# Kernel tuning notes

Measured on AMD Instinct MI355X. Metric: run time of the kernel, lower is better.

## Reference

```python
import jax, jax.numpy as jnp
import numpy as np
import math

HIDDEN = 2048
NUM_HEADS = 16
HEAD_DIM = 128
ROPE_BASE = 10000.0


def _rope_emb(seq_len, dim, dtype):
    # freqs[i, j] = i * base**(-2j/dim); emb = concat(freqs, freqs) -> [S, dim]
    inv_freq = 1.0 / (ROPE_BASE ** (jnp.arange(0, dim, 2, dtype=jnp.float32) / dim))
    t = jnp.arange(seq_len, dtype=jnp.float32)
    freqs = t[:, None] * inv_freq[None, :]            # [S, dim/2]
    return jnp.concatenate([freqs, freqs], axis=-1).astype(dtype)  # [S, dim]


def _apply_rope(x, emb):
    # x: [B, H, S, D]; emb: [S, D] broadcast over batch and heads.
    # Roll-based rotary variant from the source: x*cos + roll(x, 1, -1)*sin
    e = emb[None, None, :, :]
    return x * jnp.cos(e) + jnp.roll(x, shift=1, axis=-1) * jnp.sin(e)


def setup_inputs() -> dict:
    key = jax.random.key(0)
    ks = jax.random.split(key, 5)
    B, S = 2, 2048
    scale = 1.0 / math.sqrt(HIDDEN)
    return {
        "hidden_states": jax.random.normal(ks[0], (B, S, HIDDEN), dtype=jnp.float32),
        "Wq": jax.random.normal(ks[1], (HIDDEN, HIDDEN), dtype=jnp.float32) * scale,
        "Wk": jax.random.normal(ks[2], (HIDDEN, HIDDEN), dtype=jnp.float32) * scale,
        "Wv": jax.random.normal(ks[3], (HIDDEN, HIDDEN), dtype=jnp.float32) * scale,
        "Wo": jax.random.normal(ks[4], (HIDDEN, HIDDEN), dtype=jnp.float32) * scale,
    }


def reference(hidden_states, Wq, Wk, Wv, Wo):
    B, S, _ = hidden_states.shape
    H, D = NUM_HEADS, HEAD_DIM

    def split_heads(x):
        return x.reshape(B, S, H, D).transpose(0, 2, 1, 3)  # [B,H,S,D]

    q = split_heads(hidden_states @ Wq)
    k = split_heads(hidden_states @ Wk)
    v = split_heads(hidden_states @ Wv)

    emb = _rope_emb(S, D, hidden_states.dtype)  # [S, D]
    q = _apply_rope(q, emb)
    k = _apply_rope(k, emb)

    scores = jnp.einsum("bhqd,bhkd->bhqk", q, k) / math.sqrt(D)  # [B,H,S,S]
    probs = jax.nn.softmax(scores, axis=-1)
    ctx = jnp.einsum("bhqk,bhkd->bhqd", probs, v)  # [B,H,S,D]
    ctx = ctx.transpose(0, 2, 1, 3).reshape(B, S, H * D)
    return ctx @ Wo
```

## Files before the change

### kernel.cpp

```cpp
#include <hip/hip_runtime.h>

#define HIDDEN 2048
#define SEQ    2048
#define BATCH  2
#define NHEAD  16
#define HDIM   128

typedef __attribute__((ext_vector_type(4))) int    i32x4;
typedef __attribute__((ext_vector_type(4))) float  f32x4;
typedef __attribute__((ext_vector_type(8))) __bf16 bf16x8;

__device__ __forceinline__ unsigned short f2bf(float f) {
    return __builtin_bit_cast(unsigned short, (__bf16)f);
}
__device__ __forceinline__ float bf2f(unsigned short h) {
    unsigned u = ((unsigned)h) << 16;
    return __builtin_bit_cast(float, u);
}
__device__ __forceinline__ void gl_lds16(const unsigned short* g, unsigned short* l) {
    __builtin_amdgcn_global_load_lds(
        (const __attribute__((address_space(1))) unsigned int*)g,
        (__attribute__((address_space(3))) unsigned int*)l, 16, 0, 0);
}

__global__ void k_rope_tables(float* __restrict__ ctab, float* __restrict__ stab) {
    int idx = blockIdx.x * 256 + threadIdx.x;
    int t = idx >> 6, i = idx & 63;
    float inv = expf(-(float)i * 0.14391156831212793f);
    float ang = (float)t * inv;
    ctab[idx] = cosf(ang);
    stab[idx] = sinf(ang);
}

__global__ void k_cvt_bf16(const float* __restrict__ in, unsigned short* __restrict__ out, int n4) {
    int idx = blockIdx.x * blockDim.x + threadIdx.x;
    if (idx < n4) {
        float4 v = ((const float4*)in)[idx];
        ushort4 o;
        o.x = f2bf(v.x); o.y = f2bf(v.y); o.z = f2bf(v.z); o.w = f2bf(v.w);
        ((ushort4*)out)[idx] = o;
    }
}

__global__ void k_transcvt4(const float* __restrict__ W0, const float* __restrict__ W1,
                            const float* __restrict__ W2, const float* __restrict__ W3,
                            unsigned short* __restrict__ O0, unsigned short* __restrict__ O1,
                            unsigned short* __restrict__ O2, unsigned short* __restrict__ O3) {
    __shared__ float tile[32][33];
    int z = blockIdx.z;
    const float* in = (z == 0) ? W0 : (z == 1) ? W1 : (z == 2) ? W2 : W3;
    unsigned short* out = (z == 0) ? O0 : (z == 1) ? O1 : (z == 2) ? O2 : O3;
    float scl = (z == 0) ? 0.12751743f : 1.0f;
    int tx = threadIdx.x, ty = threadIdx.y;
    int x = blockIdx.x * 32 + tx, y0 = blockIdx.y * 32;
#pragma unroll
    for (int i = 0; i < 4; i++)
        tile[ty + i * 8][tx] = in[(size_t)(y0 + ty + i * 8) * HIDDEN + x];
    __syncthreads();
    int x2 = blockIdx.y * 32 + tx, y2 = blockIdx.x * 32;
#pragma unroll
    for (int i = 0; i < 4; i++)
        out[(size_t)(y2 + ty + i * 8) * HIDDEN + x2] = f2bf(tile[tx][ty + i * 8] * scl);
}

template <int OUTB>
__global__ __launch_bounds__(512, 1) void k_gemm256(
    const unsigned short* __restrict__ A,
    const unsigned short* __restrict__ B0, const unsigned short* __restrict__ B1,
    const unsigned short* __restrict__ B2,
    void* __restrict__ C0, void* __restrict__ C1, void* __restrict__ C2,
    int K)
{
    __shared__ __align__(16) unsigned short S[3 * 24576];
    const int nwg = gridDim.x;
    int id = blockIdx.x;
    int wg = (id & 7) * (nwg >> 3) + (id >> 3);
    const int z = wg >> 8;
    const int my = (wg >> 4) & 15, nx = wg & 15;
    const unsigned short* Bm = (z == 0) ? B0 : (z == 1 ? B1 : B2);
    void* Cv = (z == 0) ? C0 : (z == 1 ? C1 : C2);
    const int m0 = my * 256, n0 = nx * 128;
    const int tid = threadIdx.x, l = tid & 63, w = tid >> 6;
    const int wm = w >> 1, wn = w & 1;
    const int lr = l & 15, lg = l >> 4;

    const unsigned short* sg[6];
    int so[6];
#pragma unroll
    for (int j = 0; j < 4; j++) {
        int c = tid + j * 512, row = c >> 3, k8 = c & 7;
        sg[j] = A + (size_t)(m0 + row) * K + ((k8 ^ (row & 7)) * 8);
        so[j] = row * 64 + k8 * 8;
    }
#pragma unroll
    for (int j = 0; j < 2; j++) {
        int c = tid + j * 512, row = c >> 3, k8 = c & 7;
        sg[4 + j] = Bm + (size_t)(n0 + row) * K + ((k8 ^ (row & 7)) * 8);
        so[4 + j] = 16384 + row * 64 + k8 * 8;
    }

    f32x4 acc[4][4] = {};

    auto stage = [&](int t) {
        unsigned short* buf = &S[(t % 3) * 24576];
        const int ko = t * 64;
#pragma unroll
        for (int j = 0; j < 6; j++) gl_lds16(sg[j] + ko, &buf[so[j]]);
    };
    auto compute = [&](int t) {
        const unsigned short* buf = &S[(t % 3) * 24576];
        const unsigned short* bb = buf + 16384;
        const int xk0 = (lg ^ (lr & 7)) * 8, xk1 = ((4 + lg) ^ (lr & 7)) * 8;
        i32x4 af0[4], af1[4], bf0[4], bf1[4];
#pragma unroll
        for (int i = 0; i < 4; i++) {
            int R = (wm * 64 + i * 16 + lr) * 64;
            af0[i] = *(const i32x4*)&buf[R + xk0];
            af1[i] = *(const i32x4*)&buf[R + xk1];
        }
#pragma unroll
        for (int j = 0; j < 4; j++) {
            int R = (wn * 64 + j * 16 + lr) * 64;
            bf0[j] = *(const i32x4*)&bb[R + xk0];
            bf1[j] = *(const i32x4*)&bb[R + xk1];
        }
        __builtin_amdgcn_s_setprio(1);
#pragma unroll
        for (int i = 0; i < 4; i++)
#pragma unroll
            for (int j = 0; j < 4; j++)
                acc[i][j] = __builtin_amdgcn_mfma_f32_16x16x32_bf16(
                    __builtin_bit_cast(bf16x8, af0[i]),
                    __builtin_bit_cast(bf16x8, bf0[j]), acc[i][j], 0, 0, 0);
#pragma unroll
        for (int i = 0; i < 4; i++)
#pragma unroll
            for (int j = 0; j < 4; j++)
                acc[i][j] = __builtin_amdgcn_mfma_f32_16x16x32_bf16(
                    __builtin_bit_cast(bf16x8, af1[i]),
                    __builtin_bit_cast(bf16x8, bf1[j]), acc[i][j], 0, 0, 0);
        __builtin_amdgcn_s_setprio(0);
    };

    const int nt = K / 64;
    stage(0); stage(1);
    for (int t = 0; t < nt - 1; ++t) {
        asm volatile("s_waitcnt vmcnt(6)" ::: "memory");
        __builtin_amdgcn_s_barrier();
        __builtin_amdgcn_sched_barrier(0);
        if (t < nt - 2) stage(t + 2);
        compute(t);
    }
    asm volatile("s_waitcnt vmcnt(0)" ::: "memory");
    __builtin_amdgcn_s_barrier();
    __builtin_amdgcn_sched_barrier(0);
    compute(nt - 1);

#pragma unroll
    for (int i = 0; i < 4; i++)
#pragma unroll
        for (int j = 0; j < 4; j++)
#pragma unroll
            for (int r = 0; r < 4; r++) {
                int m = m0 + wm * 64 + i * 16 + lg * 4 + r;
                int n = n0 + wn * 64 + j * 16 + lr;
                float v = acc[i][j][r];
                if (OUTB) ((unsigned short*)Cv)[(size_t)m * 2048 + n] = f2bf(v);
                else      ((float*)Cv)[(size_t)m * 2048 + n] = v;
            }
}

__global__ void k_rope(unsigned short* __restrict__ Q, unsigned short* __restrict__ Kb,
                       const float* __restrict__ ctab, const float* __restrict__ stab)
{
    const int tid = threadIdx.x, l = tid & 63, w = tid >> 6;
    int hr = blockIdx.x * 4 + w;
    unsigned short* X = blockIdx.y ? Kb : Q;
    int bt = hr >> 4, h = hr & 15, t = bt & (SEQ - 1);
    size_t base = (size_t)bt * HIDDEN + h * HDIM;
    int d0 = l * 2;
    ushort2 xv = *(const ushort2*)&X[base + d0];
    float x0 = bf2f(xv.x), x1 = bf2f(xv.y);
    float prev = __shfl(x1, (l + 63) & 63);
    int i0 = d0 & 63, i1 = (d0 + 1) & 63;
    float c0 = ctab[t * 64 + i0], s0 = stab[t * 64 + i0];
    float c1 = ctab[t * 64 + i1], s1 = stab[t * 64 + i1];
    ushort2 ov;
    ov.x = f2bf(x0 * c0 + prev * s0);
    ov.y = f2bf(x1 * c1 + x0 * s1);
    *(ushort2*)&X[base + d0] = ov;
}

__global__ void k_vtrans(const unsigned short* __restrict__ V, unsigned short* __restrict__ Vt)
{
    __shared__ unsigned short tile[32][33];
    int z = blockIdx.z;
    int b = z >> 4, h = z & 15;
    int tx = threadIdx.x, ty = threadIdx.y;
    int d0 = blockIdx.x * 32, t0 = blockIdx.y * 32;
    const size_t ibase = (size_t)b * SEQ * HIDDEN + h * HDIM;
#pragma unroll
    for (int i = 0; i < 4; i++)
        tile[ty + i * 8][tx] = V[ibase + (size_t)(t0 + ty + i * 8) * HIDDEN + d0 + tx];
    __syncthreads();
    const size_t obase = (size_t)z * HDIM * SEQ;
#pragma unroll
    for (int i = 0; i < 4; i++)
        Vt[obase + (size_t)(d0 + ty + i * 8) * SEQ + t0 + tx] = tile[tx][ty + i * 8];
}

__global__ __launch_bounds__(512) void k_attn(
    const unsigned short* __restrict__ Q, const unsigned short* __restrict__ K,
    const unsigned short* __restrict__ Vt, unsigned short* __restrict__ ctx)
{
    __shared__ __align__(16) unsigned short Klds[2][64 * 128];
    __shared__ __align__(16) unsigned short Vlds[2][128 * 64];
    __shared__ __align__(16) unsigned short Plds[8][32 * 64];
    const int tid = threadIdx.x, l = tid & 63, w = tid >> 6;
    const int lr = l & 15, lg = l >> 4;
    const int bid = blockIdx.x;
    const int sX = bid >> 3;
    const int bh = (bid & 7) * 4 + (sX >> 3);
    const int q0 = (sX & 7) * 256;
    const int b = bh >> 4, h = bh & 15;

    i32x4 qf[2][4];
#pragma unroll
    for (int qh = 0; qh < 2; qh++) {
        const unsigned short* qbase =
            Q + (size_t)(b * SEQ + q0 + w * 32 + qh * 16 + lr) * HIDDEN + h * HDIM + lg * 8;
#pragma unroll
        for (int c = 0; c < 4; c++) qf[qh][c] = *(const i32x4*)(qbase + c * 32);
    }

    const unsigned short* kg[2];
    const unsigned short* vg[2];
    int kl[2], vl[2];
#pragma unroll
    for (int c = 0; c < 2; c++) {
        int cc = tid + c * 512;
        {   int row = cc >> 4, ch = cc & 15, sch = ch ^ (row & 7);
            kg[c] = K + (size_t)(b * SEQ + row) * HIDDEN + h * HDIM + sch * 8;
            kl[c] = cc * 8; }
        {   int row = cc >> 3, ch = cc & 7, sch = ch ^ (row & 7);
            vg[c] = Vt + (size_t)(bh * HDIM + row) * SEQ + sch * 8;
            vl[c] = cc * 8; }
    }

    auto stage = [&](int t, int bsel) {
        const size_t ko = (size_t)t * 64;
#pragma unroll
        for (int c = 0; c < 2; c++) {
            gl_lds16(kg[c] + ko * HIDDEN, &Klds[bsel][kl[c]]);
            gl_lds16(vg[c] + ko,          &Vlds[bsel][vl[c]]);
        }
    };

    f32x4 acc[2][8] = {};
    float m_run[2] = {-1e30f, -1e30f}, l_run[2] = {0.f, 0.f};

    stage(0, 0);
    const int nt = SEQ / 64;
    for (int t = 0; t < nt; ++t) {
        asm volatile("s_waitcnt vmcnt(0)" ::: "memory");
        __builtin_amdgcn_s_barrier();
        asm volatile("" ::: "memory");
        __builtin_amdgcn_sched_barrier(0);
        if (t + 1 < nt) stage(t + 1, (t + 1) & 1);
        const unsigned short* Kb_ = Klds[t & 1];
        const unsigned short* Vb_ = Vlds[t & 1];

        f32x4 s[4][2];
        __builtin_amdgcn_s_setprio(1);
#pragma unroll
        for (int ks = 0; ks < 4; ks++) {
            s[ks][0] = f32x4{0.f, 0.f, 0.f, 0.f};
            s[ks][1] = f32x4{0.f, 0.f, 0.f, 0.f};
#pragma unroll
            for (int c = 0; c < 4; c++) {
                i32x4 kf = *(const i32x4*)&Kb_[(ks * 16 + lr) * 128 + ((c * 4 + lg) ^ (lr & 7)) * 8];
                s[ks][0] = __builtin_amdgcn_mfma_f32_16x16x32_bf16(
                    __builtin_bit_cast(bf16x8, kf), __builtin_bit_cast(bf16x8, qf[0][c]),
                    s[ks][0], 0, 0, 0);
                s[ks][1] = __builtin_amdgcn_mfma_f32_16x16x32_bf16(
                    __builtin_bit_cast(bf16x8, kf), __builtin_bit_cast(bf16x8, qf[1][c]),
                    s[ks][1], 0, 0, 0);
            }
        }
        __builtin_amdgcn_s_setprio(0);

        float p[2][4][4];
        float fac[2];
        bool need_any = false;
#pragma unroll
        for (int qh = 0; qh < 2; qh++) {
            float mx0 = fmaxf(fmaxf(s[0][qh][0], s[0][qh][1]), fmaxf(s[0][qh][2], s[0][qh][3]));
            float mx1 = fmaxf(fmaxf(s[1][qh][0], s[1][qh][1]), fmaxf(s[1][qh][2], s[1][qh][3]));
            float mx2 = fmaxf(fmaxf(s[2][qh][0], s[2][qh][1]), fmaxf(s[2][qh][2], s[2][qh][3]));
            float mx3 = fmaxf(fmaxf(s[3][qh][0], s[3][qh][1]), fmaxf(s[3][qh][2], s[3][qh][3]));
            float pmax = fmaxf(fmaxf(mx0, mx1), fmaxf(mx2, mx3));
            pmax = fmaxf(pmax, __shfl_xor(pmax, 16));
            pmax = fmaxf(pmax, __shfl_xor(pmax, 32));
            bool need = pmax > m_run[qh] + 8.0f;
            fac[qh] = need ? __builtin_amdgcn_exp2f(m_run[qh] - pmax) : 1.0f;
            float mn = need ? pmax : m_run[qh];
            m_run[qh] = mn;
            float psum = 0.f;
#pragma unroll
            for (int ks = 0; ks < 4; ks++) {
                float e0 = __builtin_amdgcn_exp2f(s[ks][qh][0] - mn);
                float e1 = __builtin_amdgcn_exp2f(s[ks][qh][1] - mn);
                float e2 = __builtin_amdgcn_exp2f(s[ks][qh][2] - mn);
                float e3 = __builtin_amdgcn_exp2f(s[ks][qh][3] - mn);
                p[qh][ks][0] = e0; p[qh][ks][1] = e1;
                p[qh][ks][2] = e2; p[qh][ks][3] = e3;
                psum += (e0 + e1) + (e2 + e3);
            }
            psum += __shfl_xor(psum, 16);
            psum += __shfl_xor(psum, 32);
            l_run[qh] = l_run[qh] * fac[qh] + psum;
            need_any |= need;
        }

        unsigned short* pw = &Plds[w][0];
#pragma unroll
        for (int qh = 0; qh < 2; qh++)
#pragma unroll
            for (int ks = 0; ks < 4; ks++) {
                ushort4 pk;
                pk.x = f2bf(p[qh][ks][0]); pk.y = f2bf(p[qh][ks][1]);
                pk.z = f2bf(p[qh][ks][2]); pk.w = f2bf(p[qh][ks][3]);
                int chunk = ks * 2 + (lg >> 1);
                *(ushort4*)&pw[(qh * 16 + lr) * 64 + ((chunk ^ (lr & 7)) * 8) + (lg & 1) * 4] = pk;
            }

        if (__any((int)need_any)) {
#pragma unroll
            for (int qh = 0; qh < 2; qh++) {
                float facq[4];
#pragma unroll
                for (int r = 0; r < 4; r++) facq[r] = __shfl(fac[qh], lg * 4 + r);
#pragma unroll
                for (int db = 0; db < 8; db++)
#pragma unroll
                    for (int r = 0; r < 4; r++) acc[qh][db][r] *= facq[r];
            }
        }

        __builtin_amdgcn_s_setprio(1);
#pragma unroll
        for (int kk = 0; kk < 2; kk++) {
            i32x4 pf0 = *(const i32x4*)&pw[(lr) * 64 + ((kk * 4 + lg) ^ (lr & 7)) * 8];
            i32x4 pf1 = *(const i32x4*)&pw[(16 + lr) * 64 + ((kk * 4 + lg) ^ (lr & 7)) * 8];
#pragma unroll
            for (int db = 0; db < 8; db++) {
                i32x4 vf = *(const i32x4*)&Vb_[(db * 16 + lr) * 64 + ((kk * 4 + lg) ^ (lr & 7)) * 8];
                acc[0][db] = __builtin_amdgcn_mfma_f32_16x16x32_bf16(
                    __builtin_bit_cast(bf16x8, pf0), __builtin_bit_cast(bf16x8, vf),
                    acc[0][db], 0, 0, 0);
                acc[1][db] = __builtin_amdgcn_mfma_f32_16x16x32_bf16(
                    __builtin_bit_cast(bf16x8, pf1), __builtin_bit_cast(bf16x8, vf),
                    acc[1][db], 0, 0, 0);
            }
        }
        __builtin_amdgcn_s_setprio(0);
    }

#pragma unroll
    for (int qh = 0; qh < 2; qh++) {
        float inv[4];
#pragma unroll
        for (int r = 0; r < 4; r++) inv[r] = 1.0f / __shfl(l_run[qh], lg * 4 + r);
#pragma unroll
        for (int db = 0; db < 8; db++)
#pragma unroll
            for (int r = 0; r < 4; r++) {
                int trow = q0 + w * 32 + qh * 16 + lg * 4 + r;
                ctx[(size_t)(b * SEQ + trow) * HIDDEN + h * HDIM + db * 16 + lr] =
                    f2bf(acc[qh][db][r] * inv[r]);
            }
    }
}

extern "C" void kernel_launch(void* const* d_in, const int* in_sizes, int n_in,
                              void* d_out, int out_size, void* d_ws, size_t ws_size,
                              hipStream_t stream)
{
    (void)in_sizes; (void)n_in; (void)out_size; (void)ws_size;
    const float* X  = (const float*)d_in[0];
    const float* Wq = (const float*)d_in[1];
    const float* Wk = (const float*)d_in[2];
    const float* Wv = (const float*)d_in[3];
    const float* Wo = (const float*)d_in[4];
    float* out = (float*)d_out;
    char* ws = (char*)d_ws;

    unsigned short* Xb  = (unsigned short*)(ws);
    unsigned short* WqT = (unsigned short*)(ws + 16777216);
    unsigned short* WkT = (unsigned short*)(ws + 25165824);
    unsigned short* WvT = (unsigned short*)(ws + 33554432);
    unsigned short* WoT = (unsigned short*)(ws + 41943040);
    unsigned short* Qb  = (unsigned short*)(ws + 50331648);
    unsigned short* Kb  = (unsigned short*)(ws + 67108864);
    unsigned short* Vb  = (unsigned short*)(ws + 83886080);
    unsigned short* Vt  = (unsigned short*)(ws + 100663296);
    unsigned short* Cx  = (unsigned short*)(ws + 117440512);
    float* ctab = (float*)(ws + 134217728);
    float* stab = (float*)(ws + 134742016);

    k_rope_tables<<<512, 256, 0, stream>>>(ctab, stab);
    k_cvt_bf16<<<8192, 256, 0, stream>>>(X, Xb, 2097152);
    k_transcvt4<<<dim3(64, 64, 4), dim3(32, 8), 0, stream>>>(Wq, Wk, Wv, Wo,
                                                             WqT, WkT, WvT, WoT);
    k_gemm256<1><<<768, 512, 0, stream>>>(Xb, WqT, WkT, WvT, Qb, Kb, Vb, 2048);
    k_rope<<<dim3(16384, 2), 256, 0, stream>>>(Qb, Kb, ctab, stab);
    k_vtrans<<<dim3(4, 64, 32), dim3(32, 8), 0, stream>>>(Vb, Vt);
    k_attn<<<256, 512, 0, stream>>>(Qb, Kb, Vt, Cx);
    k_gemm256<0><<<256, 512, 0, stream>>>(Cx, WoT, WoT, WoT, out, out, out, 2048);
}
```

Baseline: 289.6 us.

## Split GEMM main loop into two half-phases interleaving LDS reads, prefetch and MFMA

```diff
diff --git a/kernel.cpp b/kernel.cpp
--- a/kernel.cpp
+++ b/kernel.cpp
@@ -101,19 +101,34 @@
 
     f32x4 acc[4][4] = {};
 
-    auto stage = [&](int t) {
+    auto stage6 = [&](int t) {
         unsigned short* buf = &S[(t % 3) * 24576];
         const int ko = t * 64;
 #pragma unroll
         for (int j = 0; j < 6; j++) gl_lds16(sg[j] + ko, &buf[so[j]]);
     };
-    auto compute = [&](int t) {
+    auto stageH = [&](int t, int h) {
+        unsigned short* buf = &S[(t % 3) * 24576];
+        const int ko = t * 64;
+        gl_lds16(sg[h * 2] + ko,     &buf[so[h * 2]]);
+        gl_lds16(sg[h * 2 + 1] + ko, &buf[so[h * 2 + 1]]);
+        gl_lds16(sg[4 + h] + ko,     &buf[so[4 + h]]);
+    };
+
+    const int nt = K / 64;
+    stage6(0); stage6(1);
+    asm volatile("s_waitcnt vmcnt(6)" ::: "memory");
+    __builtin_amdgcn_s_barrier();
+    __builtin_amdgcn_sched_barrier(0);
+
+    for (int t = 0; t < nt; ++t) {
         const unsigned short* buf = &S[(t % 3) * 24576];
         const unsigned short* bb = buf + 16384;
         const int xk0 = (lg ^ (lr & 7)) * 8, xk1 = ((4 + lg) ^ (lr & 7)) * 8;
-        i32x4 af0[4], af1[4], bf0[4], bf1[4];
-#pragma unroll
-        for (int i = 0; i < 4; i++) {
+        i32x4 af0[2], af1[2], bf0[4], bf1[4];
+
+#pragma unroll
+        for (int i = 0; i < 2; i++) {
             int R = (wm * 64 + i * 16 + lr) * 64;
             af0[i] = *(const i32x4*)&buf[R + xk0];
             af1[i] = *(const i32x4*)&buf[R + xk1];
@@ -124,37 +139,53 @@
             bf0[j] = *(const i32x4*)&bb[R + xk0];
             bf1[j] = *(const i32x4*)&bb[R + xk1];
         }
+        if (t + 2 < nt) stageH(t + 2, 0);
+        __builtin_amdgcn_s_barrier();
+        __builtin_amdgcn_sched_barrier(0);
         __builtin_amdgcn_s_setprio(1);
 #pragma unroll
-        for (int i = 0; i < 4; i++)
-#pragma unroll
-            for (int j = 0; j < 4; j++)
+        for (int i = 0; i < 2; i++)
+#pragma unroll
+            for (int j = 0; j < 4; j++) {
                 acc[i][j] = __builtin_amdgcn_mfma_f32_16x16x32_bf16(
                     __builtin_bit_cast(bf16x8, af0[i]),
                     __builtin_bit_cast(bf16x8, bf0[j]), acc[i][j], 0, 0, 0);
-#pragma unroll
-        for (int i = 0; i < 4; i++)
-#pragma unroll
-            for (int j = 0; j < 4; j++)
                 acc[i][j] = __builtin_amdgcn_mfma_f32_16x16x32_bf16(
                     __builtin_bit_cast(bf16x8, af1[i]),
                     __builtin_bit_cast(bf16x8, bf1[j]), acc[i][j], 0, 0, 0);
+            }
         __builtin_amdgcn_s_setprio(0);
-    };
-
-    const int nt = K / 64;
-    stage(0); stage(1);
-    for (int t = 0; t < nt - 1; ++t) {
-        asm volatile("s_waitcnt vmcnt(6)" ::: "memory");
+        __builtin_amdgcn_s_barrier();
+
+#pragma unroll
+        for (int i = 0; i < 2; i++) {
+            int R = (wm * 64 + (2 + i) * 16 + lr) * 64;
+            af0[i] = *(const i32x4*)&buf[R + xk0];
+            af1[i] = *(const i32x4*)&buf[R + xk1];
+        }
+        if (t + 2 < nt) {
+            stageH(t + 2, 1);
+            asm volatile("s_waitcnt vmcnt(6)" ::: "memory");
+        } else {
+            asm volatile("s_waitcnt vmcnt(0)" ::: "memory");
+        }
         __builtin_amdgcn_s_barrier();
         __builtin_amdgcn_sched_barrier(0);
-        if (t < nt - 2) stage(t + 2);
-        compute(t);
-    }
-    asm volatile("s_waitcnt vmcnt(0)" ::: "memory");
-    __builtin_amdgcn_s_barrier();
-    __builtin_amdgcn_sched_barrier(0);
-    compute(nt - 1);
+        __builtin_amdgcn_s_setprio(1);
+#pragma unroll
+        for (int i = 0; i < 2; i++)
+#pragma unroll
+            for (int j = 0; j < 4; j++) {
+                acc[2 + i][j] = __builtin_amdgcn_mfma_f32_16x16x32_bf16(
+                    __builtin_bit_cast(bf16x8, af0[i]),
+                    __builtin_bit_cast(bf16x8, bf0[j]), acc[2 + i][j], 0, 0, 0);
+                acc[2 + i][j] = __builtin_amdgcn_mfma_f32_16x16x32_bf16(
+                    __builtin_bit_cast(bf16x8, af1[i]),
+                    __builtin_bit_cast(bf16x8, bf1[j]), acc[2 + i][j], 0, 0, 0);
+            }
+        __builtin_amdgcn_s_setprio(0);
+        __builtin_amdgcn_s_barrier();
+    }
 
 #pragma unroll
     for (int i = 0; i < 4; i++)
```

New measurement: 296.7 us. 2.5% more time.
